# Kernel tuning notes

Measured on AMD Instinct MI355X. Metric: run time of the kernel, lower is better.

## Reference

```python
import jax, jax.numpy as jnp
import numpy as np

B, N, D = 32, 2048, 512
K = 64          # cluster_size
G = 16          # ghost_clusters
BN_EPS = 1e-5
L2_EPS = 1e-12


def setup_inputs() -> dict:
    key = jax.random.key(0)
    k1, k2, k3 = jax.random.split(key, 3)
    init_sc = 1.0 / np.sqrt(D)
    x = jax.random.normal(k1, (B, N, D), dtype=jnp.float32)
    clusters = init_sc * jax.random.normal(k2, (D, K + G), dtype=jnp.float32)
    clusters2 = init_sc * jax.random.normal(k3, (D, K), dtype=jnp.float32)
    bn_gamma = jnp.ones((K + G,), dtype=jnp.float32)
    bn_beta = jnp.zeros((K + G,), dtype=jnp.float32)
    return {"x": x, "clusters": clusters, "clusters2": clusters2,
            "bn_gamma": bn_gamma, "bn_beta": bn_beta}


def _l2norm(v, axis):
    n = jnp.sqrt(jnp.sum(v * v, axis=axis, keepdims=True))
    return v / jnp.maximum(n, L2_EPS)


def reference(x, clusters, clusters2, bn_gamma, bn_beta):
    b, n, d = x.shape
    kc = clusters2.shape[1]
    # projection: [B*N, K+G]
    a = x.reshape(-1, d) @ clusters
    # BatchNorm1d (training mode: batch statistics, biased variance)
    mean = jnp.mean(a, axis=0)
    var = jnp.mean((a - mean) ** 2, axis=0)
    a = (a - mean) * jax.lax.rsqrt(var + BN_EPS) * bn_gamma + bn_beta
    # softmax over all clusters, drop ghost clusters
    a = jax.nn.softmax(a, axis=1)[:, :kc].reshape(b, n, kc)
    # fused VLAD: v[b,d,k] = sum_n a[b,n,k] * (x[b,n,d] - c2[d,k])
    a_sum = jnp.sum(a, axis=1)                              # [B, K]
    vlad = jnp.einsum('bnd,bnk->bdk', x, a)                 # [B, D, K]
    vlad = vlad - clusters2[None, :, :] * a_sum[:, None, :]
    # intra-normalize over D, flatten, global L2 normalize
    vlad = _l2norm(vlad, axis=1)
    vlad = vlad.reshape(b, kc * d)
    vlad = _l2norm(vlad, axis=1)
    return vlad
```

## Files before the change

### kernel.cpp

```cpp
#include <hip/hip_runtime.h>
#include <hip/hip_bf16.h>

#define B_ 32
#define N_ 2048
#define D_ 512
#define KC_ 64
#define KG_ 80
#define M_ (B_*N_)

typedef __attribute__((ext_vector_type(8))) short short8;
typedef __attribute__((ext_vector_type(4))) float f32x4;

__device__ __forceinline__ unsigned short bf_rn(float f){
  unsigned int u = __float_as_uint(f);
  unsigned int r = u + 0x7FFFu + ((u >> 16) & 1u);
  return (unsigned short)(r >> 16);
}
__device__ __forceinline__ float bf_up(unsigned short h){
  return __uint_as_float(((unsigned int)h) << 16);
}
__device__ __forceinline__ void cvt8(const float* v, short8& hi, short8& lo){
#pragma unroll
  for (int i=0;i<8;i++){
    unsigned short h = bf_rn(v[i]);
    float rem = v[i] - bf_up(h);
    hi[i] = (short)h;
    lo[i] = (short)bf_rn(rem);
  }
}

__global__ __launch_bounds__(256) void k0_prep(const float* __restrict__ cl,
                                               unsigned short* __restrict__ Bf)
{
  int tid = blockIdx.x*256 + threadIdx.x;
  int l  = tid & 63;
  int hl = (tid >> 6) & 1;
  int j  = (tid >> 7) % 5;
  int c  = tid / 640;
  int kk  = c*32 + (l>>4)*8;
  int col = j*16 + (l&15);
  unsigned short o[8];
#pragma unroll
  for (int jj=0;jj<8;jj++){
    float v = cl[(size_t)(kk+jj)*KG_ + col];
    unsigned short h = bf_rn(v);
    if (hl == 0) o[jj] = h;
    else         o[jj] = bf_rn(v - bf_up(h));
  }
#pragma unroll
  for (int jj=0;jj<8;jj++) Bf[(size_t)tid*8 + jj] = o[jj];
}

__global__ __launch_bounds__(256) void k1_proj(
    const float* __restrict__ x, const unsigned short* __restrict__ Bf,
    float* __restrict__ a, float* __restrict__ S1, float* __restrict__ S2)
{
  __shared__ float ls1[KG_], ls2[KG_];
  const int t = threadIdx.x;
  const int w = t >> 6, lane = t & 63;
  const int m = lane & 15, q = lane >> 4;
  const int row0 = blockIdx.x*128 + w*32;
  if (t < KG_){ ls1[t]=0.f; ls2[t]=0.f; }

  const float* xr0 = x + (size_t)(row0 + m)*D_ + q*8;
  const float* xr1 = xr0 + (size_t)16*D_;

  f32x4 acc[2][5];
#pragma unroll
  for (int rt=0;rt<2;rt++)
#pragma unroll
    for (int j=0;j<5;j++) acc[rt][j] = (f32x4){0.f,0.f,0.f,0.f};

  for (int c=0;c<16;c++){
    float v0[8], v1[8];
    *(float4*)&v0[0] = *(const float4*)(xr0 + c*32);
    *(float4*)&v0[4] = *(const float4*)(xr0 + c*32 + 4);
    *(float4*)&v1[0] = *(const float4*)(xr1 + c*32);
    *(float4*)&v1[4] = *(const float4*)(xr1 + c*32 + 4);
    short8 ah0, al0, ah1, al1;
    cvt8(v0, ah0, al0);
    cvt8(v1, ah1, al1);
    const unsigned short* bp = Bf + (size_t)(c*5)*1024 + lane*8;
#pragma unroll
    for (int j=0;j<5;j++){
      short8 bhi = *(const short8*)(bp + (size_t)j*1024);
      short8 blo = *(const short8*)(bp + (size_t)j*1024 + 512);
      acc[0][j] = __builtin_amdgcn_mfma_f32_16x16x32_bf16(ah0, bhi, acc[0][j], 0,0,0);
      acc[0][j] = __builtin_amdgcn_mfma_f32_16x16x32_bf16(al0, bhi, acc[0][j], 0,0,0);
      acc[0][j] = __builtin_amdgcn_mfma_f32_16x16x32_bf16(ah0, blo, acc[0][j], 0,0,0);
      acc[1][j] = __builtin_amdgcn_mfma_f32_16x16x32_bf16(ah1, bhi, acc[1][j], 0,0,0);
      acc[1][j] = __builtin_amdgcn_mfma_f32_16x16x32_bf16(al1, bhi, acc[1][j], 0,0,0);
      acc[1][j] = __builtin_amdgcn_mfma_f32_16x16x32_bf16(ah1, blo, acc[1][j], 0,0,0);
    }
  }

  float s1v[5] = {0,0,0,0,0}, s2v[5] = {0,0,0,0,0};
#pragma unroll
  for (int rt=0;rt<2;rt++){
#pragma unroll
    for (int j=0;j<5;j++){
      f32x4 v = acc[rt][j];
      size_t base = (size_t)(row0 + rt*16 + q*4)*KG_ + j*16 + m;
      a[base]        = v[0];
      a[base+KG_]    = v[1];
      a[base+2*KG_]  = v[2];
      a[base+3*KG_]  = v[3];
      s1v[j] += v[0]+v[1]+v[2]+v[3];
      s2v[j] += v[0]*v[0]+v[1]*v[1]+v[2]*v[2]+v[3]*v[3];
    }
  }
#pragma unroll
  for (int j=0;j<5;j++){
    float s1 = s1v[j], s2 = s2v[j];
    s1 += __shfl_xor(s1,16); s1 += __shfl_xor(s1,32);
    s2 += __shfl_xor(s2,16); s2 += __shfl_xor(s2,32);
    if (q == 0){
      atomicAdd(&ls1[j*16+m], s1);
      atomicAdd(&ls2[j*16+m], s2);
    }
  }
  __syncthreads();
  if (t < KG_){ atomicAdd(&S1[t], ls1[t]); atomicAdd(&S2[t], ls2[t]); }
}

__global__ void k2_bn(const float* __restrict__ S1, const float* __restrict__ S2,
                      const float* __restrict__ gamma, const float* __restrict__ beta,
                      float* __restrict__ scale, float* __restrict__ shift)
{
  int t = threadIdx.x;
  if (t < KG_){
    const float invM = 1.0f / (float)M_;
    float mean = S1[t] * invM;
    float var  = S2[t] * invM - mean*mean;
    float sc = gamma[t] * rsqrtf(var + 1e-5f);
    scale[t] = sc;
    shift[t] = beta[t] - mean*sc;
  }
}

__global__ __launch_bounds__(256) void k3_softmax(
    float* __restrict__ a, const float* __restrict__ scale,
    const float* __restrict__ shift, float* __restrict__ asum)
{
  __shared__ float as[64*84];
  __shared__ float sc[KG_], sh[KG_];
  __shared__ float lsum[KC_];
  const int t = threadIdx.x;
  const int row0 = blockIdx.x * 64;
  if (t < KG_){ sc[t]=scale[t]; sh[t]=shift[t]; }
  if (t < KC_) lsum[t]=0.f;
  __syncthreads();
#pragma unroll
  for (int l=0;l<20;l++){
    int idx = t + 256*l;
    int r = idx/80, col = idx - r*80;
    float v = a[(size_t)(row0+r)*KG_ + col];
    as[r*84+col] = v*sc[col] + sh[col];
  }
  __syncthreads();
  const int rt = t >> 2;
  const int g  = t & 3;
  float m = -1e30f;
#pragma unroll
  for (int c=0;c<20;c++) m = fmaxf(m, as[rt*84 + g + 4*c]);
  m = fmaxf(m, __shfl_xor(m,1));
  m = fmaxf(m, __shfl_xor(m,2));
  float e[20]; float s = 0.f;
#pragma unroll
  for (int c=0;c<20;c++){ float v = __expf(as[rt*84 + g + 4*c] - m); e[c]=v; s+=v; }
  s += __shfl_xor(s,1);
  s += __shfl_xor(s,2);
  const float inv = 1.f/s;
#pragma unroll
  for (int c=0;c<16;c++){
    int col = g + 4*c;
    float pv = e[c]*inv;
    a[(size_t)(row0+rt)*KG_ + col] = pv;
    float su = pv;
    su += __shfl_xor(su,4);  su += __shfl_xor(su,8);
    su += __shfl_xor(su,16); su += __shfl_xor(su,32);
    if ((t&63) < 4) atomicAdd(&lsum[col], su);
  }
  __syncthreads();
  if (t < KC_) atomicAdd(&asum[(blockIdx.x>>5)*KC_ + t], lsum[t]);
}

__global__ __launch_bounds__(256) void k4_vlad(
    const float* __restrict__ x, const float* __restrict__ p, float* __restrict__ vp)
{
  __shared__ unsigned short xh[64*40], xl[64*40];
  __shared__ unsigned short ph[64*40], pl[64*40];
  const int t = threadIdx.x;
  const int blk = blockIdx.x;
  const int ns = blk & 3;
  const int dt = (blk >> 2) & 7;
  const int b  = blk >> 5;
  const int w = t >> 6, lane = t & 63;
  const int m = lane & 15, q = lane >> 4;
  const int d0 = dt*64;
  const int nbase = ns*512;
  const int dloc = t & 63, ng = t >> 6;

  f32x4 acc[4];
#pragma unroll
  for (int j=0;j<4;j++) acc[j] = (f32x4){0.f,0.f,0.f,0.f};

  for (int n0=0;n0<512;n0+=32){
    {
      float v[8];
      const float* xp = x + ((size_t)b*N_ + nbase + n0 + ng*8)*D_ + d0 + dloc;
#pragma unroll
      for (int jj=0;jj<8;jj++) v[jj] = xp[(size_t)jj*D_];
      short8 hi, lo; cvt8(v, hi, lo);
      *(short8*)&xh[dloc*40 + ng*8] = hi;
      *(short8*)&xl[dloc*40 + ng*8] = lo;
    }
    {
      float v[8];
      const float* pp = p + ((size_t)b*N_ + nbase + n0 + ng*8)*KG_ + dloc;
#pragma unroll
      for (int jj=0;jj<8;jj++) v[jj] = pp[(size_t)jj*KG_];
      short8 hi, lo; cvt8(v, hi, lo);
      *(short8*)&ph[dloc*40 + ng*8] = hi;
      *(short8*)&pl[dloc*40 + ng*8] = lo;
    }
    __syncthreads();
    short8 ahi = *(const short8*)&xh[(w*16+m)*40 + q*8];
    short8 alo = *(const short8*)&xl[(w*16+m)*40 + q*8];
#pragma unroll
    for (int j=0;j<4;j++){
      short8 bhi = *(const short8*)&ph[(j*16+m)*40 + q*8];
      short8 blo = *(const short8*)&pl[(j*16+m)*40 + q*8];
      acc[j] = __builtin_amdgcn_mfma_f32_16x16x32_bf16(ahi, bhi, acc[j], 0,0,0);
      acc[j] = __builtin_amdgcn_mfma_f32_16x16x32_bf16(alo, bhi, acc[j], 0,0,0);
      acc[j] = __builtin_amdgcn_mfma_f32_16x16x32_bf16(ahi, blo, acc[j], 0,0,0);
    }
    __syncthreads();
  }
#pragma unroll
  for (int j=0;j<4;j++){
    f32x4 v = acc[j];
    size_t base = (((size_t)ns*B_ + b)*D_ + d0 + w*16 + q*4)*KC_ + j*16 + m;
    vp[base]         = v[0];
    vp[base +   KC_] = v[1];
    vp[base + 2*KC_] = v[2];
    vp[base + 3*KC_] = v[3];
  }
}

__global__ __launch_bounds__(1024) void k5_norm(
    const float* __restrict__ vp, const float* __restrict__ c2,
    const float* __restrict__ asum, float* __restrict__ out)
{
  __shared__ float part[16][64];
  __shared__ float invd[64];
  __shared__ float gi_s;
  const int b = blockIdx.x;
  const int t = threadIdx.x;
  const int k = t & 63, dg = t >> 6;
  const float av = asum[b*KC_ + k];
  const size_t stride = (size_t)B_*D_*KC_;
  float v[32];
  float ss = 0.f;
#pragma unroll
  for (int s=0;s<32;s++){
    int d = dg + 16*s;
    size_t idx = ((size_t)b*D_ + d)*KC_ + k;
    float vv = 0.f;
#pragma unroll
    for (int nsp=0;nsp<4;nsp++) vv += vp[idx + (size_t)nsp*stride];
    vv -= c2[d*KC_ + k]*av;
    v[s] = vv;
    ss += vv*vv;
  }
  part[dg][k] = ss;
  __syncthreads();
  if (t < 64){
    float n2 = 0.f;
#pragma unroll
    for (int i=0;i<16;i++) n2 += part[i][t];
    float nn = sqrtf(n2);
    float denom = fmaxf(nn, 1e-12f);
    invd[t] = 1.f/denom;
    float ratio = nn/denom;
    float r2 = ratio*ratio;
#pragma unroll
    for (int mm=1;mm<64;mm<<=1) r2 += __shfl_xor(r2, mm);
    if (t==0){
      float g = sqrtf(r2);
      gi_s = 1.f/fmaxf(g, 1e-12f);
    }
  }
  __syncthreads();
  const float gi = gi_s;
  const float ik = invd[k];
#pragma unroll
  for (int s=0;s<32;s++){
    int d = dg + 16*s;
    out[(size_t)b*(D_*KC_) + (size_t)d*KC_ + k] = v[s]*ik*gi;
  }
}

extern "C" void kernel_launch(void* const* d_in, const int* in_sizes, int n_in,
                              void* d_out, int out_size, void* d_ws, size_t ws_size,
                              hipStream_t stream)
{
  const float* x     = (const float*)d_in[0];
  const float* cl    = (const float*)d_in[1];
  const float* c2    = (const float*)d_in[2];
  const float* gamma = (const float*)d_in[3];
  const float* beta  = (const float*)d_in[4];
  float* out = (float*)d_out;
  float* ws  = (float*)d_ws;

  float* S1    = ws;
  float* S2    = ws + 80;
  float* scale = ws + 160;
  float* shift = ws + 240;
  float* asum  = ws + 320;
  unsigned short* Bf = (unsigned short*)(ws + 4096);
  float* a     = ws + 45056;
  float* vp    = a + (size_t)M_*KG_;

  hipMemsetAsync(ws, 0, 2368*sizeof(float), stream);
  k0_prep   <<<40,   256, 0, stream>>>(cl, Bf);
  k1_proj   <<<512,  256, 0, stream>>>(x, Bf, a, S1, S2);
  k2_bn     <<<1,    128, 0, stream>>>(S1, S2, gamma, beta, scale, shift);
  k3_softmax<<<1024, 256, 0, stream>>>(a, scale, shift, asum);
  k4_vlad   <<<1024, 256, 0, stream>>>(x, a, vp);
  k5_norm   <<<32,  1024, 0, stream>>>(vp, c2, asum, out);
}
```

Before: 276.2 us.

## Prefetch and double-buffer operands in projection and VLAD kernels, halve projection tile

```diff
diff --git a/kernel.cpp b/kernel.cpp
--- a/kernel.cpp
+++ b/kernel.cpp
@@ -59,55 +59,58 @@
   const int t = threadIdx.x;
   const int w = t >> 6, lane = t & 63;
   const int m = lane & 15, q = lane >> 4;
-  const int row0 = blockIdx.x*128 + w*32;
+  const int row0 = blockIdx.x*64 + w*16;
   if (t < KG_){ ls1[t]=0.f; ls2[t]=0.f; }
-
-  const float* xr0 = x + (size_t)(row0 + m)*D_ + q*8;
-  const float* xr1 = xr0 + (size_t)16*D_;
-
-  f32x4 acc[2][5];
-#pragma unroll
-  for (int rt=0;rt<2;rt++)
-#pragma unroll
-    for (int j=0;j<5;j++) acc[rt][j] = (f32x4){0.f,0.f,0.f,0.f};
+  __syncthreads();
+
+  const float* xr = x + (size_t)(row0 + m)*D_ + q*8;
+
+  f32x4 acc[5];
+#pragma unroll
+  for (int j=0;j<5;j++) acc[j] = (f32x4){0.f,0.f,0.f,0.f};
+
+  float v[8];
+  *(float4*)&v[0] = *(const float4*)(xr);
+  *(float4*)&v[4] = *(const float4*)(xr + 4);
 
   for (int c=0;c<16;c++){
-    float v0[8], v1[8];
-    *(float4*)&v0[0] = *(const float4*)(xr0 + c*32);
-    *(float4*)&v0[4] = *(const float4*)(xr0 + c*32 + 4);
-    *(float4*)&v1[0] = *(const float4*)(xr1 + c*32);
-    *(float4*)&v1[4] = *(const float4*)(xr1 + c*32 + 4);
-    short8 ah0, al0, ah1, al1;
-    cvt8(v0, ah0, al0);
-    cvt8(v1, ah1, al1);
+    float nv[8];
+    if (c < 15){
+      *(float4*)&nv[0] = *(const float4*)(xr + (c+1)*32);
+      *(float4*)&nv[4] = *(const float4*)(xr + (c+1)*32 + 4);
+    }
     const unsigned short* bp = Bf + (size_t)(c*5)*1024 + lane*8;
+    short8 bh[5], bl[5];
 #pragma unroll
     for (int j=0;j<5;j++){
-      short8 bhi = *(const short8*)(bp + (size_t)j*1024);
-      short8 blo = *(const short8*)(bp + (size_t)j*1024 + 512);
-      acc[0][j] = __builtin_amdgcn_mfma_f32_16x16x32_bf16(ah0, bhi, acc[0][j], 0,0,0);
-      acc[0][j] = __builtin_amdgcn_mfma_f32_16x16x32_bf16(al0, bhi, acc[0][j], 0,0,0);
-      acc[0][j] = __builtin_amdgcn_mfma_f32_16x16x32_bf16(ah0, blo, acc[0][j], 0,0,0);
-      acc[1][j] = __builtin_amdgcn_mfma_f32_16x16x32_bf16(ah1, bhi, acc[1][j], 0,0,0);
-      acc[1][j] = __builtin_amdgcn_mfma_f32_16x16x32_bf16(al1, bhi, acc[1][j], 0,0,0);
-      acc[1][j] = __builtin_amdgcn_mfma_f32_16x16x32_bf16(ah1, blo, acc[1][j], 0,0,0);
-    }
-  }
-
-  float s1v[5] = {0,0,0,0,0}, s2v[5] = {0,0,0,0,0};
-#pragma unroll
-  for (int rt=0;rt<2;rt++){
+      bh[j] = *(const short8*)(bp + (size_t)j*1024);
+      bl[j] = *(const short8*)(bp + (size_t)j*1024 + 512);
+    }
+    short8 ah, al;
+    cvt8(v, ah, al);
 #pragma unroll
     for (int j=0;j<5;j++){
-      f32x4 v = acc[rt][j];
-      size_t base = (size_t)(row0 + rt*16 + q*4)*KG_ + j*16 + m;
-      a[base]        = v[0];
-      a[base+KG_]    = v[1];
-      a[base+2*KG_]  = v[2];
-      a[base+3*KG_]  = v[3];
-      s1v[j] += v[0]+v[1]+v[2]+v[3];
-      s2v[j] += v[0]*v[0]+v[1]*v[1]+v[2]*v[2]+v[3]*v[3];
-    }
+      acc[j] = __builtin_amdgcn_mfma_f32_16x16x32_bf16(ah, bh[j], acc[j], 0,0,0);
+      acc[j] = __builtin_amdgcn_mfma_f32_16x16x32_bf16(al, bh[j], acc[j], 0,0,0);
+      acc[j] = __builtin_amdgcn_mfma_f32_16x16x32_bf16(ah, bl[j], acc[j], 0,0,0);
+    }
+    if (c < 15){
+#pragma unroll
+      for (int i=0;i<8;i++) v[i] = nv[i];
+    }
+  }
+
+  float s1v[5], s2v[5];
+#pragma unroll
+  for (int j=0;j<5;j++){
+    f32x4 vv = acc[j];
+    size_t base = (size_t)(row0 + q*4)*KG_ + j*16 + m;
+    a[base]        = vv[0];
+    a[base+KG_]    = vv[1];
+    a[base+2*KG_]  = vv[2];
+    a[base+3*KG_]  = vv[3];
+    s1v[j] = vv[0]+vv[1]+vv[2]+vv[3];
+    s2v[j] = vv[0]*vv[0]+vv[1]*vv[1]+vv[2]*vv[2]+vv[3]*vv[3];
   }
 #pragma unroll
   for (int j=0;j<5;j++){
@@ -188,8 +191,8 @@
 __global__ __launch_bounds__(256) void k4_vlad(
     const float* __restrict__ x, const float* __restrict__ p, float* __restrict__ vp)
 {
-  __shared__ unsigned short xh[64*40], xl[64*40];
-  __shared__ unsigned short ph[64*40], pl[64*40];
+  __shared__ unsigned short xh[2][64*40], xl[2][64*40];
+  __shared__ unsigned short ph[2][64*40], pl[2][64*40];
   const int t = threadIdx.x;
   const int blk = blockIdx.x;
   const int ns = blk & 3;
@@ -201,39 +204,60 @@
   const int nbase = ns*512;
   const int dloc = t & 63, ng = t >> 6;
 
+  const float* xbase = x + ((size_t)b*N_ + nbase)*D_ + d0 + dloc;
+  const float* pbase = p + ((size_t)b*N_ + nbase)*KG_ + dloc;
+
   f32x4 acc[4];
 #pragma unroll
   for (int j=0;j<4;j++) acc[j] = (f32x4){0.f,0.f,0.f,0.f};
 
-  for (int n0=0;n0<512;n0+=32){
-    {
-      float v[8];
-      const float* xp = x + ((size_t)b*N_ + nbase + n0 + ng*8)*D_ + d0 + dloc;
-#pragma unroll
-      for (int jj=0;jj<8;jj++) v[jj] = xp[(size_t)jj*D_];
-      short8 hi, lo; cvt8(v, hi, lo);
-      *(short8*)&xh[dloc*40 + ng*8] = hi;
-      *(short8*)&xl[dloc*40 + ng*8] = lo;
-    }
-    {
-      float v[8];
-      const float* pp = p + ((size_t)b*N_ + nbase + n0 + ng*8)*KG_ + dloc;
-#pragma unroll
-      for (int jj=0;jj<8;jj++) v[jj] = pp[(size_t)jj*KG_];
-      short8 hi, lo; cvt8(v, hi, lo);
-      *(short8*)&ph[dloc*40 + ng*8] = hi;
-      *(short8*)&pl[dloc*40 + ng*8] = lo;
-    }
-    __syncthreads();
-    short8 ahi = *(const short8*)&xh[(w*16+m)*40 + q*8];
-    short8 alo = *(const short8*)&xl[(w*16+m)*40 + q*8];
+  {
+    float xv[8], pv[8];
+#pragma unroll
+    for (int jj=0;jj<8;jj++){
+      xv[jj] = xbase[(size_t)(ng*8+jj)*D_];
+      pv[jj] = pbase[(size_t)(ng*8+jj)*KG_];
+    }
+    short8 hi, lo;
+    cvt8(xv, hi, lo);
+    *(short8*)&xh[0][dloc*40 + ng*8] = hi;
+    *(short8*)&xl[0][dloc*40 + ng*8] = lo;
+    cvt8(pv, hi, lo);
+    *(short8*)&ph[0][dloc*40 + ng*8] = hi;
+    *(short8*)&pl[0][dloc*40 + ng*8] = lo;
+  }
+  __syncthreads();
+
+  for (int ch=0; ch<16; ch++){
+    const int cur = ch & 1;
+    float nxv[8], npv[8];
+    if (ch < 15){
+      const float* xp2 = xbase + (size_t)((ch+1)*32)*D_;
+      const float* pp2 = pbase + (size_t)((ch+1)*32)*KG_;
+#pragma unroll
+      for (int jj=0;jj<8;jj++){
+        nxv[jj] = xp2[(size_t)(ng*8+jj)*D_];
+        npv[jj] = pp2[(size_t)(ng*8+jj)*KG_];
+      }
+    }
+    short8 ahi = *(const short8*)&xh[cur][(w*16+m)*40 + q*8];
+    short8 alo = *(const short8*)&xl[cur][(w*16+m)*40 + q*8];
 #pragma unroll
     for (int j=0;j<4;j++){
-      short8 bhi = *(const short8*)&ph[(j*16+m)*40 + q*8];
-      short8 blo = *(const short8*)&pl[(j*16+m)*40 + q*8];
+      short8 bhi = *(const short8*)&ph[cur][(j*16+m)*40 + q*8];
+      short8 blo = *(const short8*)&pl[cur][(j*16+m)*40 + q*8];
       acc[j] = __builtin_amdgcn_mfma_f32_16x16x32_bf16(ahi, bhi, acc[j], 0,0,0);
       acc[j] = __builtin_amdgcn_mfma_f32_16x16x32_bf16(alo, bhi, acc[j], 0,0,0);
       acc[j] = __builtin_amdgcn_mfma_f32_16x16x32_bf16(ahi, blo, acc[j], 0,0,0);
+    }
+    if (ch < 15){
+      short8 hi, lo;
+      cvt8(nxv, hi, lo);
+      *(short8*)&xh[cur^1][dloc*40 + ng*8] = hi;
+      *(short8*)&xl[cur^1][dloc*40 + ng*8] = lo;
+      cvt8(npv, hi, lo);
+      *(short8*)&ph[cur^1][dloc*40 + ng*8] = hi;
+      *(short8*)&pl[cur^1][dloc*40 + ng*8] = lo;
     }
     __syncthreads();
   }
@@ -324,7 +348,7 @@
 
   hipMemsetAsync(ws, 0, 2368*sizeof(float), stream);
   k0_prep   <<<40,   256, 0, stream>>>(cl, Bf);
-  k1_proj   <<<512,  256, 0, stream>>>(x, Bf, a, S1, S2);
+  k1_proj   <<<1024, 256, 0, stream>>>(x, Bf, a, S1, S2);
   k2_bn     <<<1,    128, 0, stream>>>(S1, S2, gamma, beta, scale, shift);
   k3_softmax<<<1024, 256, 0, stream>>>(a, scale, shift, asum);
   k4_vlad   <<<1024, 256, 0, stream>>>(x, a, vp);
```

Result: slower. 292.2 us (+5.8%).
